# Optimization experiments

Hardware: AMD Instinct MI355X
Metric: run time of the kernel (lower is better)

The kernel has to match this reference:

```python
import jax, jax.numpy as jnp
import numpy as np
import math

H, HK, D = 16, 4, 128  # n_heads, n_kv_heads, head_dim
WINDOW = 1024
ROPE_BASE = 10000.0
EPS = 1e-6

def _rope_cos_sin(T, dtype):
    inv_freq = 1.0 / (ROPE_BASE ** (jnp.arange(0, D, 2, dtype=jnp.float32) / D))
    ang = jnp.arange(T, dtype=jnp.float32)[:, None] * inv_freq[None, :]  # [T, D/2]
    cos = jnp.concatenate([jnp.cos(ang), jnp.cos(ang)], axis=-1)  # [T, D]
    sin = jnp.concatenate([jnp.sin(ang), jnp.sin(ang)], axis=-1)
    return cos.astype(dtype), sin.astype(dtype)

def _rotate_half(x):
    x1, x2 = jnp.split(x, 2, axis=-1)
    return jnp.concatenate([-x2, x1], axis=-1)

def _apply_rope(t, cos, sin):
    # t: [B, h, T, D]; cos/sin: [T, D]
    return t * cos[None, None] + _rotate_half(t) * sin[None, None]

def setup_inputs() -> dict:
    key = jax.random.key(0)
    ks = jax.random.split(key, 7)
    d = H * D
    s = 1.0 / math.sqrt(d)
    return {
        "x": jax.random.normal(ks[0], (2, 2048, d), jnp.float32),
        "wq": jax.random.normal(ks[1], (H * D, d), jnp.float32) * s,
        "wk": jax.random.normal(ks[2], (HK * D, d), jnp.float32) * s,
        "wv": jax.random.normal(ks[3], (HK * D, d), jnp.float32) * s,
        "wo": jax.random.normal(ks[4], (d, H * D), jnp.float32) * s,
        "gamma_q": jnp.ones((D,), jnp.float32),
        "gamma_k": jnp.ones((D,), jnp.float32),
    }

def reference(x, wq, wk, wv, wo, gamma_q, gamma_k):
    B, T, d = x.shape
    G = H // HK  # query heads per kv head
    # projections (Linear stores [out, in]) -> [B, h, T, D]
    q = jnp.einsum('btd,ed->bte', x, wq).reshape(B, T, H, D).transpose(0, 2, 1, 3)
    k = jnp.einsum('btd,ed->bte', x, wk).reshape(B, T, HK, D).transpose(0, 2, 1, 3)
    v = jnp.einsum('btd,ed->bte', x, wv).reshape(B, T, HK, D).transpose(0, 2, 1, 3)
    cos, sin = _rope_cos_sin(T, x.dtype)
    q = _apply_rope(q, cos, sin)
    k = _apply_rope(k, cos, sin)
    # QK-norm: L2 normalize then learned per-dim scale
    q = q / (jnp.linalg.norm(q, axis=-1, keepdims=True) + EPS) * gamma_q
    k = k / (jnp.linalg.norm(k, axis=-1, keepdims=True) + EPS) * gamma_k
    # GQA: group query heads instead of materializing repeated K/V
    qg = q.reshape(B, HK, G, T, D)
    att = jnp.einsum('bkgtd,bksd->bkgts', qg, k) / math.sqrt(D)  # [B,HK,G,T,T]
    i = jnp.arange(T)
    diff = i[:, None] - i[None, :]
    bad = (diff < 0) | (diff > WINDOW)  # causal OR beyond sliding window
    att = jnp.where(bad[None, None, None], -jnp.inf, att)
    p = jax.nn.softmax(att, axis=-1)
    y = jnp.einsum('bkgts,bksd->bkgtd', p, v)  # [B,HK,G,T,D]
    y = y.reshape(B, H, T, D).transpose(0, 2, 1, 3).reshape(B, T, H * D)
    y = jnp.einsum('bte,de->btd', y, wo)
    return y
```

## Files before the change

### kernel.cpp

```cpp
#include <hip/hip_runtime.h>
#include <cstdint>
#include <cstddef>

typedef unsigned short u16;
typedef short bf16x8 __attribute__((ext_vector_type(8)));
typedef float f32x4 __attribute__((ext_vector_type(4)));

#define MFMA(a,b,c) __builtin_amdgcn_mfma_f32_16x16x32_bf16(a,b,c,0,0,0)

__device__ __forceinline__ u16 f2bf(float f) {
  unsigned u = __builtin_bit_cast(unsigned, f);
  u += 0x7fffu + ((u >> 16) & 1u);
  return (u16)(u >> 16);
}
__device__ __forceinline__ float bf2f(u16 b) {
  return __builtin_bit_cast(float, (unsigned)b << 16);
}
__device__ __forceinline__ float exp2_hw(float x) {
  float r;
  asm("v_exp_f32 %0, %1" : "=v"(r) : "v"(x));
  return r;
}
__device__ __forceinline__ void gl_lds16(const void* g, void* l) {
  __builtin_amdgcn_global_load_lds(
      (const __attribute__((address_space(1))) void*)g,
      (__attribute__((address_space(3))) void*)l, 16, 0, 0);
}
template <int N>
__device__ __forceinline__ void wait_vmcnt() {
  if constexpr (N == 0) asm volatile("s_waitcnt vmcnt(0)" ::: "memory");
  else if constexpr (N == 4) asm volatile("s_waitcnt vmcnt(4)" ::: "memory");
  else if constexpr (N == 6) asm volatile("s_waitcnt vmcnt(6)" ::: "memory");
  else if constexpr (N == 8) asm volatile("s_waitcnt vmcnt(8)" ::: "memory");
}

__global__ __launch_bounds__(256) void cvt_all(const float* __restrict__ x,
                                               const float* __restrict__ wq,
                                               const float* __restrict__ wk,
                                               const float* __restrict__ wv,
                                               const float* __restrict__ wo,
                                               u16* __restrict__ xb,
                                               u16* __restrict__ wqkvb,
                                               u16* __restrict__ wob) {
  int idx = (blockIdx.x * 256 + threadIdx.x) * 4;
  const float* src;
  u16* dst;
  if (idx < 8388608) { src = x + idx; dst = xb + idx; }
  else if (idx < 12582912) { src = wq + (idx - 8388608); dst = wqkvb + (idx - 8388608); }
  else if (idx < 13631488) { src = wk + (idx - 12582912); dst = wqkvb + (idx - 8388608); }
  else if (idx < 14680064) { src = wv + (idx - 13631488); dst = wqkvb + (idx - 8388608); }
  else if (idx < 18874368) { src = wo + (idx - 14680064); dst = wob + (idx - 14680064); }
  else return;
  float4 v = *(const float4*)src;
  ushort4 o = {f2bf(v.x), f2bf(v.y), f2bf(v.z), f2bf(v.w)};
  *(ushort4*)dst = o;
}

__global__ __launch_bounds__(256) void rope_table(float* __restrict__ ctab,
                                                  float* __restrict__ stab) {
  int i = blockIdx.x * 256 + threadIdx.x;
  int t = i >> 6, f = i & 63;
  float inv_freq = powf(10000.0f, -(2.0f * f) / 128.0f);
  float ang = (float)t * inv_freq;
  ctab[i] = cosf(ang);
  stab[i] = sinf(ang);
}

template <int BM, int BN, int OUT_F32>
__global__ __launch_bounds__(512, 2) void gemm8p(const u16* __restrict__ A,
                                                 const u16* __restrict__ Bw,
                                                 void* __restrict__ Cout,
                                                 int M, int N, int K) {
  constexpr int WN = BN / 64;
  constexpr int WM = 8 / WN;
  constexpr int MSUB = BM / WM;
  constexpr int MF = MSUB / 16;
  constexpr int CHA = BM / 8;
  constexpr int CPW = (CHA + BN / 8) / 8;

  __shared__ u16 As[2][BM * 64];
  __shared__ u16 Bs[2][BN * 64];
  const int tid = threadIdx.x;
  const int lane = tid & 63;
  const int wv = tid >> 6;
  const int l16 = lane & 15, lhi = lane >> 4;
  const int wm = wv / WN, wn = wv % WN;
  const int m0 = blockIdx.y * BM;
  const int n0 = blockIdx.x * BN;
  const int nt = K >> 6;

  const int srow8 = lane >> 3;
  const int scol = ((lane & 7) * 16) ^ (srow8 << 4);

  auto stage_tile = [&](int buf, int kt) {
#pragma unroll
    for (int c = 0; c < CPW; ++c) {
      int g = wv + 8 * c;
      if (g < CHA) {
        int row = m0 + g * 8 + srow8;
        const char* src = (const char*)A + ((size_t)row * K + (size_t)kt * 64) * 2 + scol;
        gl_lds16(src, (char*)As[buf] + g * 1024);
      } else {
        int gb = g - CHA;
        int row = n0 + gb * 8 + srow8;
        const char* src = (const char*)Bw + ((size_t)row * K + (size_t)kt * 64) * 2 + scol;
        gl_lds16(src, (char*)Bs[buf] + gb * 1024);
      }
    }
  };
  auto readA = [&](int buf, int mi, int kk) -> bf16x8 {
    int lr = wm * MSUB + mi * 16 + l16;
    return *(const bf16x8*)((const char*)As[buf] + lr * 128 +
                            ((kk * 64 + lhi * 16) ^ ((l16 & 7) << 4)));
  };
  auto readB = [&](int buf, int ni, int kk) -> bf16x8 {
    int lr = wn * 64 + ni * 16 + l16;
    return *(const bf16x8*)((const char*)Bs[buf] + lr * 128 +
                            ((kk * 64 + lhi * 16) ^ ((l16 & 7) << 4)));
  };

  f32x4 acc[MF][4] = {};

  stage_tile(0, 0);
  stage_tile(1, 1);
  wait_vmcnt<CPW>();
  __builtin_amdgcn_sched_barrier(0);
  __builtin_amdgcn_s_barrier();
  __builtin_amdgcn_sched_barrier(0);

  for (int t = 0; t < nt; ++t) {
    const int b = t & 1;
    bf16x8 bf0[4], af0[MF];
#pragma unroll
    for (int ni = 0; ni < 4; ++ni) bf0[ni] = readB(b, ni, 0);
#pragma unroll
    for (int mi = 0; mi < MF; ++mi) af0[mi] = readA(b, mi, 0);
    __builtin_amdgcn_s_setprio(1);
#pragma unroll
    for (int mi = 0; mi < MF; ++mi)
#pragma unroll
      for (int ni = 0; ni < 4; ++ni)
        acc[mi][ni] = MFMA(af0[mi], bf0[ni], acc[mi][ni]);
    __builtin_amdgcn_s_setprio(0);
    bf16x8 bf1[4], af1[MF];
#pragma unroll
    for (int ni = 0; ni < 4; ++ni) bf1[ni] = readB(b, ni, 1);
#pragma unroll
    for (int mi = 0; mi < MF; ++mi) af1[mi] = readA(b, mi, 1);
    asm volatile("s_waitcnt lgkmcnt(0)" ::: "memory");
    __builtin_amdgcn_sched_barrier(0);
    __builtin_amdgcn_s_barrier();
    __builtin_amdgcn_sched_barrier(0);
    if (t + 2 < nt) stage_tile(b, t + 2);
    __builtin_amdgcn_s_setprio(1);
#pragma unroll
    for (int mi = 0; mi < MF; ++mi)
#pragma unroll
      for (int ni = 0; ni < 4; ++ni)
        acc[mi][ni] = MFMA(af1[mi], bf1[ni], acc[mi][ni]);
    __builtin_amdgcn_s_setprio(0);
    if (t + 2 < nt) wait_vmcnt<CPW>();
    else if (t + 1 < nt) wait_vmcnt<0>();
    __builtin_amdgcn_sched_barrier(0);
    __builtin_amdgcn_s_barrier();
    __builtin_amdgcn_sched_barrier(0);
  }

#pragma unroll
  for (int mi = 0; mi < MF; ++mi)
#pragma unroll
    for (int ni = 0; ni < 4; ++ni) {
      int col = n0 + wn * 64 + ni * 16 + l16;
#pragma unroll
      for (int j = 0; j < 4; ++j) {
        int row = m0 + wm * MSUB + mi * 16 + lhi * 4 + j;
        float v = acc[mi][ni][j];
        if (OUT_F32)
          ((float*)Cout)[(size_t)row * N + col] = v;
        else
          ((u16*)Cout)[(size_t)row * N + col] = f2bf(v);
      }
    }
}

template <int NH>
__global__ __launch_bounds__(256) void rope_norm(const u16* __restrict__ raw,
                                                 u16* __restrict__ out,
                                                 const float* __restrict__ ctab,
                                                 const float* __restrict__ stab,
                                                 const float* __restrict__ gamma,
                                                 int stride, int coloff, float scale) {
  int gw = blockIdx.x * 4 + (threadIdx.x >> 6);
  int lane = threadIdx.x & 63;
  int h = gw & (NH - 1);
  int bt = gw / NH;
  int t = bt & 2047, bb = bt >> 11;
  const u16* r = raw + (size_t)bt * stride + coloff + (size_t)h * 128;
  ushort2 own = *(const ushort2*)(r + 2 * lane);
  int pk = __shfl_xor(__builtin_bit_cast(int, own), 32);
  ushort2 par = __builtin_bit_cast(ushort2, pk);
  float x0 = bf2f(own.x), x1 = bf2f(own.y);
  float y0 = bf2f(par.x), y1 = bf2f(par.y);
  int f = (lane & 31) * 2;
  float2 c2 = *(const float2*)(ctab + t * 64 + f);
  float2 s2 = *(const float2*)(stab + t * 64 + f);
  bool hi = lane >= 32;
  float e0 = hi ? (x0 * c2.x + y0 * s2.x) : (x0 * c2.x - y0 * s2.x);
  float e1 = hi ? (x1 * c2.y + y1 * s2.y) : (x1 * c2.y - y1 * s2.y);
  float ss = e0 * e0 + e1 * e1;
#pragma unroll
  for (int off = 1; off < 64; off <<= 1) ss += __shfl_xor(ss, off);
  float inv = scale / (sqrtf(ss) + 1e-6f);
  float2 g2 = *(const float2*)(gamma + 2 * lane);
  size_t ob = (((size_t)(bb * NH + h)) * 2048 + t) * 128 + 2 * lane;
  ushort2 o = {f2bf(e0 * inv * g2.x), f2bf(e1 * inv * g2.y)};
  *(ushort2*)(out + ob) = o;
}

__global__ __launch_bounds__(256) void transpose_v(const u16* __restrict__ qkv,
                                                   u16* __restrict__ vt) {
  __shared__ u16 tile[32][33];
  int t0 = blockIdx.x * 32, d0 = blockIdx.y * 32;
  int bh = blockIdx.z;
  int b = bh >> 2, hkk = bh & 3;
  int tx = threadIdx.x & 31, ty = threadIdx.x >> 5;
#pragma unroll
  for (int i = 0; i < 4; ++i) {
    int r = ty + i * 8;
    tile[r][tx] = qkv[((size_t)(b * 2048 + t0 + r)) * 3072 + 2560 + hkk * 128 + d0 + tx];
  }
  __syncthreads();
#pragma unroll
  for (int i = 0; i < 4; ++i) {
    int r = ty + i * 8;
    vt[((size_t)((b * 4 + hkk) * 128 + d0 + r)) * 2048 + t0 + tx] = tile[tx][r];
  }
}

__global__ __launch_bounds__(512, 4) void attn_kernel(const u16* __restrict__ Qr,
                                                      const u16* __restrict__ Kr,
                                                      const u16* __restrict__ Vt,
                                                      u16* __restrict__ Yt) {
  __shared__ u16 Ks[2][64 * 128];
  __shared__ u16 Vs[2][128 * 64];
  __shared__ u16 Ps[8][16 * 64];
  const int tid = threadIdx.x;
  const int lane = tid & 63;
  const int wv = tid >> 6;
  const int l16 = lane & 15, lhi = lane >> 4;
  const int work = (blockIdx.x & 7) * 64 + (blockIdx.x >> 3);
  const int q0b = (work & 15) << 7;
  const int bh = work >> 4;
  const int b = bh >> 4, h = bh & 15;
  const int hk = h >> 2;
  const int q0w = q0b + wv * 16;

  const u16* qbase = Qr + (((size_t)bh) * 2048 + q0w + l16) * 128;
  bf16x8 qf[4];
#pragma unroll
  for (int dc = 0; dc < 4; ++dc)
    qf[dc] = *(const bf16x8*)(qbase + dc * 32 + lhi * 8);

  const char* kg = (const char*)(Kr + ((size_t)(b * 4 + hk)) * 2048 * 128);
  const u16* vg = Vt + ((size_t)(b * 4 + hk)) * 2048 * 128;

  auto stage = [&](int buf, int s0) {
#pragma unroll
    for (int i = 0; i < 2; ++i) {
      int c = wv + 8 * i;
      int row = c * 4 + lhi;
      int srcb = (l16 * 16) ^ ((row & 7) << 4);
      gl_lds16(kg + (size_t)(s0 + row) * 256 + srcb, (char*)Ks[buf] + c * 1024);
    }
    int r8 = lane >> 3, c8 = lane & 7;
#pragma unroll
    for (int i = 0; i < 2; ++i) {
      int c = wv + 8 * i;
      int row = c * 8 + r8;
      int srcb = (c8 * 16) ^ ((r8 & 7) << 4);
      gl_lds16((const char*)(vg + (size_t)row * 2048 + s0) + srcb,
               (char*)Vs[buf] + c * 1024);
    }
  };

  const bf16x8 ones = {0x3F80, 0x3F80, 0x3F80, 0x3F80, 0x3F80, 0x3F80, 0x3F80, 0x3F80};
  float mbase = 0.f;
  f32x4 lacc = {};
  f32x4 oacc[8] = {};

  int s_lo = q0b - 1024; if (s_lo < 0) s_lo = 0;
  const int nt = (q0b + 128 - s_lo) >> 6;

  stage(0, s_lo);
  int cur = 0;
  for (int it = 0; it < nt; ++it) {
    const int s0 = s_lo + (it << 6);
    if (it + 1 < nt) {
      stage(cur ^ 1, s0 + 64);
      wait_vmcnt<4>();
    } else {
      wait_vmcnt<0>();
    }
    __builtin_amdgcn_sched_barrier(0);
    __builtin_amdgcn_s_barrier();
    __builtin_amdgcn_sched_barrier(0);
    const bool skip = (q0w + 15 < s0) || (q0w - (s0 + 63) > 1024);
    if (!skip) {
      f32x4 sacc[4] = {};
      const char* ksb = (const char*)Ks[cur];
      __builtin_amdgcn_s_setprio(1);
#pragma unroll
      for (int n = 0; n < 4; ++n) {
        int row = n * 16 + l16;
#pragma unroll
        for (int dc = 0; dc < 4; ++dc) {
          bf16x8 kf = *(const bf16x8*)(ksb + row * 256 +
                                       ((dc * 64 + lhi * 16) ^ ((l16 & 7) << 4)));
          sacc[n] = MFMA(qf[dc], kf, sacc[n]);
        }
      }
      __builtin_amdgcn_s_setprio(0);
      const bool domask = (q0w < s0 + 63) || (q0w + 15 - s0 > 1024);
      if (domask) {
#pragma unroll
        for (int n = 0; n < 4; ++n)
#pragma unroll
          for (int j = 0; j < 4; ++j) {
            int q = q0w + lhi * 4 + j;
            int s = s0 + n * 16 + l16;
            if ((unsigned)(q - s) > 1024u) sacc[n][j] = -INFINITY;
          }
      }
      float mt = sacc[0][0];
#pragma unroll
      for (int n = 0; n < 4; ++n)
#pragma unroll
        for (int j = 0; j < 4; ++j) mt = fmaxf(mt, sacc[n][j]);
#pragma unroll
      for (int off = 1; off < 64; off <<= 1) mt = fmaxf(mt, __shfl_xor(mt, off));
      if (mt > mbase + 8.f) {
        float sc2 = exp2_hw(mbase - mt);
#pragma unroll
        for (int j = 0; j < 4; ++j) lacc[j] *= sc2;
#pragma unroll
        for (int dt = 0; dt < 8; ++dt)
#pragma unroll
          for (int j = 0; j < 4; ++j) oacc[dt][j] *= sc2;
        mbase = mt;
      }
      char* psb = (char*)Ps[wv];
#pragma unroll
      for (int n = 0; n < 4; ++n)
#pragma unroll
        for (int j = 0; j < 4; ++j) {
          float p = exp2_hw(sacc[n][j] - mbase);
          int R = lhi * 4 + j;
          *(u16*)(psb + R * 128 + (((n * 16 + l16) * 2) ^ ((R & 7) << 4))) = f2bf(p);
        }
      bf16x8 pf[2];
#pragma unroll
      for (int kk = 0; kk < 2; ++kk)
        pf[kk] = *(const bf16x8*)(psb + l16 * 128 +
                                  ((kk * 64 + lhi * 16) ^ ((l16 & 7) << 4)));
      const char* vsb = (const char*)Vs[cur];
      __builtin_amdgcn_s_setprio(1);
      lacc = MFMA(pf[0], ones, lacc);
      lacc = MFMA(pf[1], ones, lacc);
#pragma unroll
      for (int dt = 0; dt < 8; ++dt) {
        int row = dt * 16 + l16;
#pragma unroll
        for (int kk = 0; kk < 2; ++kk) {
          bf16x8 vf = *(const bf16x8*)(vsb + row * 128 +
                                       ((kk * 64 + lhi * 16) ^ ((l16 & 7) << 4)));
          oacc[dt] = MFMA(pf[kk], vf, oacc[dt]);
        }
      }
      __builtin_amdgcn_s_setprio(0);
    }
    __builtin_amdgcn_sched_barrier(0);
    __builtin_amdgcn_s_barrier();
    __builtin_amdgcn_sched_barrier(0);
    cur ^= 1;
  }
#pragma unroll
  for (int j = 0; j < 4; ++j) {
    float inv = 1.0f / lacc[j];
    int q = q0w + lhi * 4 + j;
    size_t rowbase = ((size_t)(b * 2048 + q)) * 2048 + (size_t)h * 128;
#pragma unroll
    for (int dt = 0; dt < 8; ++dt)
      Yt[rowbase + dt * 16 + l16] = f2bf(oacc[dt][j] * inv);
  }
}

extern "C" void kernel_launch(void* const* d_in, const int* in_sizes, int n_in,
                              void* d_out, int out_size, void* d_ws, size_t ws_size,
                              hipStream_t stream) {
  (void)in_sizes; (void)n_in; (void)out_size; (void)ws_size;
  const float* x  = (const float*)d_in[0];
  const float* wq = (const float*)d_in[1];
  const float* wk = (const float*)d_in[2];
  const float* wv = (const float*)d_in[3];
  const float* wo = (const float*)d_in[4];
  const float* gq = (const float*)d_in[5];
  const float* gk = (const float*)d_in[6];
  float* out = (float*)d_out;
  char* ws = (char*)d_ws;

  size_t off = 0;
  auto alloc = [&](size_t bytes) {
    size_t o = off;
    off += (bytes + 255) & ~(size_t)255;
    return o;
  };
  u16* xb     = (u16*)(ws + alloc((size_t)4096 * 2048 * 2));
  u16* wqkvb  = (u16*)(ws + alloc((size_t)3072 * 2048 * 2));
  u16* wob    = (u16*)(ws + alloc((size_t)2048 * 2048 * 2));
  u16* qkvraw = (u16*)(ws + alloc((size_t)4096 * 3072 * 2));
  u16* qr     = (u16*)(ws + alloc((size_t)4096 * 2048 * 2));
  u16* kr     = (u16*)(ws + alloc((size_t)4096 * 512 * 2));
  u16* vt     = (u16*)(ws + alloc((size_t)4096 * 512 * 2));
  float* ctab = (float*)(ws + alloc((size_t)2048 * 64 * 4));
  float* stab = (float*)(ws + alloc((size_t)2048 * 64 * 4));
  u16* ytmp = qkvraw;

  const float sc_log2 = 0.12751744f;

  cvt_all<<<18432, 256, 0, stream>>>(x, wq, wk, wv, wo, xb, wqkvb, wob);
  rope_table<<<512, 256, 0, stream>>>(ctab, stab);

  gemm8p<256, 256, 0><<<dim3(12, 16), 512, 0, stream>>>(xb, wqkvb, qkvraw, 4096, 3072, 2048);

  rope_norm<16><<<16384, 256, 0, stream>>>(qkvraw, qr, ctab, stab, gq, 3072, 0, sc_log2);
  rope_norm<4><<<4096, 256, 0, stream>>>(qkvraw, kr, ctab, stab, gk, 3072, 2048, 1.0f);
  transpose_v<<<dim3(64, 4, 8), 256, 0, stream>>>(qkvraw, vt);

  attn_kernel<<<dim3(512), 512, 0, stream>>>(qr, kr, vt, ytmp);

  gemm8p<256, 128, 1><<<dim3(16, 16), 512, 0, stream>>>(ytmp, wob, out, 4096, 2048, 2048);
}
```

Baseline: 198.4 us.

## Load GEMM B operand directly to registers with prefetch instead of LDS

Replaces LDS staging of the weight (B) tile with direct global-to-register loads, double-buffered one k-tile ahead. Only A still goes through LDS via global_load_lds. This cuts LDS footprint and LDS read traffic and halves the staging work. In exchange it adds register pressure and strided, less coalesced global loads that rely on L2 for reuse across waves.

```diff
diff --git a/kernel.cpp b/kernel.cpp
--- a/kernel.cpp
+++ b/kernel.cpp
@@ -30,8 +30,8 @@
 __device__ __forceinline__ void wait_vmcnt() {
   if constexpr (N == 0) asm volatile("s_waitcnt vmcnt(0)" ::: "memory");
   else if constexpr (N == 4) asm volatile("s_waitcnt vmcnt(4)" ::: "memory");
-  else if constexpr (N == 6) asm volatile("s_waitcnt vmcnt(6)" ::: "memory");
   else if constexpr (N == 8) asm volatile("s_waitcnt vmcnt(8)" ::: "memory");
+  else if constexpr (N == 12) asm volatile("s_waitcnt vmcnt(12)" ::: "memory");
 }
 
 __global__ __launch_bounds__(256) void cvt_all(const float* __restrict__ x,
@@ -67,19 +67,18 @@
 }
 
 template <int BM, int BN, int OUT_F32>
-__global__ __launch_bounds__(512, 2) void gemm8p(const u16* __restrict__ A,
-                                                 const u16* __restrict__ Bw,
-                                                 void* __restrict__ Cout,
-                                                 int M, int N, int K) {
+__global__ __launch_bounds__(512, 2) void gemm_bs(const u16* __restrict__ A,
+                                                  const u16* __restrict__ Bw,
+                                                  void* __restrict__ Cout,
+                                                  int M, int N, int K) {
   constexpr int WN = BN / 64;
   constexpr int WM = 8 / WN;
   constexpr int MSUB = BM / WM;
   constexpr int MF = MSUB / 16;
-  constexpr int CHA = BM / 8;
-  constexpr int CPW = (CHA + BN / 8) / 8;
+  constexpr int APW = BM / 8 / 8;
 
   __shared__ u16 As[2][BM * 64];
-  __shared__ u16 Bs[2][BN * 64];
+
   const int tid = threadIdx.x;
   const int lane = tid & 63;
   const int wv = tid >> 6;
@@ -92,20 +91,13 @@
   const int srow8 = lane >> 3;
   const int scol = ((lane & 7) * 16) ^ (srow8 << 4);
 
-  auto stage_tile = [&](int buf, int kt) {
-#pragma unroll
-    for (int c = 0; c < CPW; ++c) {
+  auto stageA = [&](int buf, int kt) {
+#pragma unroll
+    for (int c = 0; c < APW; ++c) {
       int g = wv + 8 * c;
-      if (g < CHA) {
-        int row = m0 + g * 8 + srow8;
-        const char* src = (const char*)A + ((size_t)row * K + (size_t)kt * 64) * 2 + scol;
-        gl_lds16(src, (char*)As[buf] + g * 1024);
-      } else {
-        int gb = g - CHA;
-        int row = n0 + gb * 8 + srow8;
-        const char* src = (const char*)Bw + ((size_t)row * K + (size_t)kt * 64) * 2 + scol;
-        gl_lds16(src, (char*)Bs[buf] + gb * 1024);
-      }
+      int row = m0 + g * 8 + srow8;
+      const char* src = (const char*)A + ((size_t)row * K + (size_t)kt * 64) * 2 + scol;
+      gl_lds16(src, (char*)As[buf] + g * 1024);
     }
   };
   auto readA = [&](int buf, int mi, int kk) -> bf16x8 {
@@ -113,57 +105,62 @@
     return *(const bf16x8*)((const char*)As[buf] + lr * 128 +
                             ((kk * 64 + lhi * 16) ^ ((l16 & 7) << 4)));
   };
-  auto readB = [&](int buf, int ni, int kk) -> bf16x8 {
-    int lr = wn * 64 + ni * 16 + l16;
-    return *(const bf16x8*)((const char*)Bs[buf] + lr * 128 +
-                            ((kk * 64 + lhi * 16) ^ ((l16 & 7) << 4)));
+  const u16* bbase = Bw + (size_t)(n0 + wn * 64 + l16) * K + lhi * 8;
+  auto loadB = [&](int kt, int ni, int kk) -> bf16x8 {
+    return *(const bf16x8*)(bbase + (size_t)(ni * 16) * K + kt * 64 + kk * 32);
   };
 
   f32x4 acc[MF][4] = {};
-
-  stage_tile(0, 0);
-  stage_tile(1, 1);
-  wait_vmcnt<CPW>();
+  bf16x8 bc[2][4], bn[2][4];
+
+  stageA(0, 0);
+  stageA(1, 1);
+#pragma unroll
+  for (int kk = 0; kk < 2; ++kk)
+#pragma unroll
+    for (int ni = 0; ni < 4; ++ni) bc[kk][ni] = loadB(0, ni, kk);
+  wait_vmcnt<12>();
   __builtin_amdgcn_sched_barrier(0);
   __builtin_amdgcn_s_barrier();
   __builtin_amdgcn_sched_barrier(0);
 
-  for (int t = 0; t < nt; ++t) {
+  auto body = [&](int t, bf16x8 (*bcur)[4], bf16x8 (*bnext)[4]) {
     const int b = t & 1;
-    bf16x8 bf0[4], af0[MF];
-#pragma unroll
-    for (int ni = 0; ni < 4; ++ni) bf0[ni] = readB(b, ni, 0);
-#pragma unroll
-    for (int mi = 0; mi < MF; ++mi) af0[mi] = readA(b, mi, 0);
+    if (t + 1 < nt) {
+#pragma unroll
+      for (int kk = 0; kk < 2; ++kk)
+#pragma unroll
+        for (int ni = 0; ni < 4; ++ni) bnext[kk][ni] = loadB(t + 1, ni, kk);
+    }
     __builtin_amdgcn_s_setprio(1);
 #pragma unroll
-    for (int mi = 0; mi < MF; ++mi)
-#pragma unroll
-      for (int ni = 0; ni < 4; ++ni)
-        acc[mi][ni] = MFMA(af0[mi], bf0[ni], acc[mi][ni]);
+    for (int kk = 0; kk < 2; ++kk)
+#pragma unroll
+      for (int mi = 0; mi < MF; ++mi) {
+        bf16x8 a = readA(b, mi, kk);
+#pragma unroll
+        for (int ni = 0; ni < 4; ++ni)
+          acc[mi][ni] = MFMA(a, bcur[kk][ni], acc[mi][ni]);
+      }
     __builtin_amdgcn_s_setprio(0);
-    bf16x8 bf1[4], af1[MF];
-#pragma unroll
-    for (int ni = 0; ni < 4; ++ni) bf1[ni] = readB(b, ni, 1);
-#pragma unroll
-    for (int mi = 0; mi < MF; ++mi) af1[mi] = readA(b, mi, 1);
     asm volatile("s_waitcnt lgkmcnt(0)" ::: "memory");
     __builtin_amdgcn_sched_barrier(0);
     __builtin_amdgcn_s_barrier();
     __builtin_amdgcn_sched_barrier(0);
-    if (t + 2 < nt) stage_tile(b, t + 2);
-    __builtin_amdgcn_s_setprio(1);
-#pragma unroll
-    for (int mi = 0; mi < MF; ++mi)
-#pragma unroll
-      for (int ni = 0; ni < 4; ++ni)
-        acc[mi][ni] = MFMA(af1[mi], bf1[ni], acc[mi][ni]);
-    __builtin_amdgcn_s_setprio(0);
-    if (t + 2 < nt) wait_vmcnt<CPW>();
-    else if (t + 1 < nt) wait_vmcnt<0>();
+    if (t + 2 < nt) {
+      stageA(b, t + 2);
+      wait_vmcnt<12>();
+    } else if (t + 1 < nt) {
+      wait_vmcnt<8>();
+    }
     __builtin_amdgcn_sched_barrier(0);
     __builtin_amdgcn_s_barrier();
     __builtin_amdgcn_sched_barrier(0);
+  };
+
+  for (int t = 0; t < nt; t += 2) {
+    body(t, bc, bn);
+    body(t + 1, bn, bc);
   }
 
 #pragma unroll
@@ -430,7 +427,7 @@
   cvt_all<<<18432, 256, 0, stream>>>(x, wq, wk, wv, wo, xb, wqkvb, wob);
   rope_table<<<512, 256, 0, stream>>>(ctab, stab);
 
-  gemm8p<256, 256, 0><<<dim3(12, 16), 512, 0, stream>>>(xb, wqkvb, qkvraw, 4096, 3072, 2048);
+  gemm_bs<256, 256, 0><<<dim3(12, 16), 512, 0, stream>>>(xb, wqkvb, qkvraw, 4096, 3072, 2048);
 
   rope_norm<16><<<16384, 256, 0, stream>>>(qkvraw, qr, ctab, stab, gq, 3072, 0, sc_log2);
   rope_norm<4><<<4096, 256, 0, stream>>>(qkvraw, kr, ctab, stab, gk, 3072, 2048, 1.0f);
@@ -438,5 +435,5 @@
 
   attn_kernel<<<dim3(512), 512, 0, stream>>>(qr, kr, vt, ytmp);
 
-  gemm8p<256, 128, 1><<<dim3(16, 16), 512, 0, stream>>>(ytmp, wob, out, 4096, 2048, 2048);
-}
+  gemm_bs<256, 128, 1><<<dim3(16, 16), 512, 0, stream>>>(ytmp, wob, out, 4096, 2048, 2048);
+}
```

After: 362.6 us. 82.8% more time.
